# Optimization experiments

Hardware: AMD Instinct MI355X
Metric: run time of the kernel (lower is better)

## Reference

```python
import jax, jax.numpy as jnp
import numpy as np

EPS_BN = 1e-5
NEG_SLOPE = 0.2

def gat_layer(x, src, dst, N, W, a_src, a_dst, b, heads, ch, concat):
    # x: [N, Fin]; W: [Fin, heads*ch]; a_src/a_dst: [heads, ch]; b: [heads*ch] or [ch]
    xw = (x @ W).reshape(N, heads, ch)                      # [N,H,C]
    al_src = jnp.einsum('nhc,hc->nh', xw, a_src)            # [N,H]
    al_dst = jnp.einsum('nhc,hc->nh', xw, a_dst)
    e = jax.nn.leaky_relu(al_src[src] + al_dst[dst], NEG_SLOPE)  # [E,H]
    m = jax.ops.segment_max(e, dst, num_segments=N)         # segment softmax (stable)
    ee = jnp.exp(e - m[dst])
    s = jax.ops.segment_sum(ee, dst, num_segments=N)
    alpha = ee / (s[dst] + 1e-16)                            # [E,H]
    msg = xw[src] * alpha[:, :, None]                        # [E,H,C]
    out = jax.ops.segment_sum(msg, dst, num_segments=N)      # [N,H,C]
    if concat:
        return out.reshape(N, heads * ch) + b
    return out.mean(axis=1) + b

def setup_inputs():
    key = jax.random.key(0)
    ks = jax.random.split(key, 24)
    N, E, dim_in, dim_out = 20000, 320000, 256, 16
    x = jax.random.normal(ks[0], (N, dim_in), dtype=jnp.float32)
    edge_index = jax.random.randint(ks[1], (2, E), 0, N, dtype=jnp.int64)
    def glorot(k, shape):
        fan = shape[0] + shape[-1]
        return jax.random.uniform(k, shape, jnp.float32, -1.0, 1.0) * np.sqrt(6.0 / fan)
    return {
        'x': x, 'edge_index': edge_index,
        'bn_gamma': jnp.ones((dim_in,), jnp.float32),
        'bn_beta': jnp.zeros((dim_in,), jnp.float32),
        'W1': glorot(ks[2], (dim_in, 16 * 64)),
        'a1_src': glorot(ks[3], (16, 64)), 'a1_dst': glorot(ks[4], (16, 64)),
        'b1': jnp.zeros((16 * 64,), jnp.float32),
        'p1': jnp.float32(0.25),
        'W2': glorot(ks[5], (dim_in + 16 * 64, 8 * 8)),
        'a2_src': glorot(ks[6], (8, 8)), 'a2_dst': glorot(ks[7], (8, 8)),
        'b2': jnp.zeros((8 * 8,), jnp.float32),
        'p2': jnp.float32(0.25),
        'W3': glorot(ks[8], (8 * 8, 8 * dim_out)),
        'a3_src': glorot(ks[9], (8, dim_out)), 'a3_dst': glorot(ks[10], (8, dim_out)),
        'b3': jnp.zeros((dim_out,), jnp.float32),
    }

def reference(x, edge_index, bn_gamma, bn_beta, W1, a1_src, a1_dst, b1, p1,
              W2, a2_src, a2_dst, b2, p2, W3, a3_src, a3_dst, b3):
    N = x.shape[0]
    # PyG GATConv default add_self_loops=True
    loops = jnp.arange(N, dtype=edge_index.dtype)
    src = jnp.concatenate([edge_index[0], loops])
    dst = jnp.concatenate([edge_index[1], loops])
    # BatchNorm1d (training-mode batch stats)
    mu = x.mean(axis=0)
    var = x.var(axis=0)
    x_in = (x - mu) * jax.lax.rsqrt(var + EPS_BN) * bn_gamma + bn_beta
    h = gat_layer(x_in, src, dst, N, W1, a1_src, a1_dst, b1, 16, 64, True)
    h = jnp.where(h >= 0, h, p1 * h)  # PReLU
    h = gat_layer(jnp.concatenate([x_in, h], axis=1), src, dst, N, W2, a2_src, a2_dst, b2, 8, 8, True)
    h = jnp.where(h >= 0, h, p2 * h)
    h = gat_layer(h, src, dst, N, W3, a3_src, a3_dst, b3, 8, b3.shape[0], False)
    return jax.nn.log_softmax(h, axis=1)
```

## Files before the change

### kernel.cpp

```cpp
#include <hip/hip_runtime.h>
#include <math.h>

typedef unsigned int u32;
typedef unsigned short u16;
typedef u32 u32x4 __attribute__((ext_vector_type(4)));
typedef float f32x4 __attribute__((ext_vector_type(4)));

__device__ __forceinline__ u16 f2bf(float f) {
  u32 u = __builtin_bit_cast(u32, f);
  return (u16)((u + 0x7FFFu + ((u >> 16) & 1u)) >> 16);
}
__device__ __forceinline__ float bf2f(u32 lo16) {
  return __builtin_bit_cast(float, lo16 << 16);
}
__device__ __forceinline__ void mfma16(f32x4& c, const u32x4& a, const u32x4& b) {
  asm volatile("v_mfma_f32_16x16x32_bf16 %0, %1, %2, %0" : "+v"(c) : "v"(a), "v"(b));
}
__device__ __forceinline__ float lrelu(float e) { return fmaxf(e, 0.2f * e); }

__global__ void bn_stats_kernel(const float* __restrict__ x, float* __restrict__ musum,
                                float* __restrict__ sqsum, int N, int F) {
  int t = threadIdx.x;
  float s = 0.f, s2 = 0.f;
  for (int r = blockIdx.x; r < N; r += gridDim.x) {
    float v = x[(size_t)r * F + t];
    s += v;
    s2 += v * v;
  }
  atomicAdd(&musum[t], s);
  atomicAdd(&sqsum[t], s2);
}

__global__ void bn_finalize_kernel(const float* __restrict__ musum, const float* __restrict__ sqsum,
                                   const float* __restrict__ gamma, const float* __restrict__ beta,
                                   float* __restrict__ scale, float* __restrict__ shift, int N) {
  int t = threadIdx.x;
  float m = musum[t] / (float)N;
  float v = sqsum[t] / (float)N - m * m;
  float sc = gamma[t] * rsqrtf(v + 1e-5f);
  scale[t] = sc;
  shift[t] = beta[t] - m * sc;
}

__global__ void bn_apply_bf16_kernel(const float* __restrict__ x, const float* __restrict__ scale,
                                     const float* __restrict__ shift, u16* __restrict__ xin,
                                     int total, int Fmask) {
  int i = blockIdx.x * blockDim.x + threadIdx.x;
  if (i < total) {
    int c = i & Fmask;
    xin[i] = f2bf(x[i] * scale[c] + shift[c]);
  }
}

__global__ void csr_count_kernel(const int* __restrict__ ei, int E, int N, int* __restrict__ cnt) {
  int e = blockIdx.x * blockDim.x + threadIdx.x;
  int ET = E + N;
  if (e < ET) {
    int d = (e < E) ? ei[E + e] : (e - E);
    atomicAdd(&cnt[d], 1);
  }
}

__global__ __launch_bounds__(1024) void csr_scan_kernel(const int* __restrict__ cnt,
                                                        int* __restrict__ row_ptr,
                                                        int* __restrict__ cursor, int N) {
  __shared__ int part[1024];
  int t = threadIdx.x;
  int chunk = (N + 1023) / 1024;
  int lo = t * chunk;
  int hi = min(lo + chunk, N);
  int s = 0;
  for (int i = lo; i < hi; i++) s += cnt[i];
  part[t] = s;
  __syncthreads();
  for (int off = 1; off < 1024; off <<= 1) {
    int v = (t >= off) ? part[t - off] : 0;
    __syncthreads();
    part[t] += v;
    __syncthreads();
  }
  int run = (t == 0) ? 0 : part[t - 1];
  for (int i = lo; i < hi; i++) {
    row_ptr[i] = run;
    cursor[i] = run;
    run += cnt[i];
  }
  if (t == 1023) row_ptr[N] = part[1023];
}

__global__ void csr_fill_kernel(const int* __restrict__ ei, int E, int N,
                                int* __restrict__ cursor, int* __restrict__ csr_src) {
  int e = blockIdx.x * blockDim.x + threadIdx.x;
  int ET = E + N;
  if (e < ET) {
    int s, d;
    if (e < E) { s = ei[e]; d = ei[E + e]; }
    else       { s = e - E; d = s; }
    int pos = atomicAdd(&cursor[d], 1);
    csr_src[pos] = s;
  }
}

__global__ void wt_build_all(const float* __restrict__ W1, const float* __restrict__ W2,
                             const float* __restrict__ W3, u16* __restrict__ Wt1,
                             u16* __restrict__ Wt2, u16* __restrict__ Wt3) {
  const int S1 = 1024 * 256, S2 = 64 * 1280, S3 = 128 * 64;
  const int P1 = 96 * 256, P2 = 32 * 1280, P3 = 32 * 64;
  int idx = blockIdx.x * blockDim.x + threadIdx.x;
  if (idx < S1) {
    int n = idx / 256, k = idx % 256;
    Wt1[idx] = f2bf(W1[(size_t)k * 1024 + n]);
  } else if (idx < S1 + S2) {
    int i = idx - S1;
    int n = i / 1280, k = i % 1280;
    Wt2[i] = f2bf(W2[(size_t)k * 64 + n]);
  } else if (idx < S1 + S2 + S3) {
    int i = idx - S1 - S2;
    int n = i / 64, k = i % 64;
    Wt3[i] = f2bf(W3[(size_t)k * 128 + n]);
  } else if (idx < S1 + S2 + S3 + P1) {
    Wt1[S1 + (idx - S1 - S2 - S3)] = 0;
  } else if (idx < S1 + S2 + S3 + P1 + P2) {
    Wt2[S2 + (idx - S1 - S2 - S3 - P1)] = 0;
  } else if (idx < S1 + S2 + S3 + P1 + P2 + P3) {
    Wt3[S3 + (idx - S1 - S2 - S3 - P1 - P2)] = 0;
  }
}

__global__ void alfold_build(const float* __restrict__ W1, const float* __restrict__ a1s,
                             const float* __restrict__ a1d, const float* __restrict__ W2,
                             const float* __restrict__ a2s, const float* __restrict__ a2d,
                             const float* __restrict__ W3, const float* __restrict__ a3s,
                             const float* __restrict__ a3d, u16* __restrict__ Wt1,
                             u16* __restrict__ Wt2, u16* __restrict__ Wt3) {
  const int T1 = 32 * 256, T2 = 16 * 1280, T3 = 16 * 64;
  int idx = blockIdx.x * blockDim.x + threadIdx.x;
  if (idx < T1) {
    int jj = idx / 256, k = idx % 256, h = jj >> 1;
    const float* av = (jj & 1) ? a1d : a1s;
    float s = 0.f;
    for (int c = 0; c < 64; c++) s += W1[(size_t)k * 1024 + h * 64 + c] * av[h * 64 + c];
    Wt1[(size_t)(1024 + jj) * 256 + k] = f2bf(s);
  } else if (idx < T1 + T2) {
    int i = idx - T1;
    int jj = i / 1280, k = i % 1280, h = jj >> 1;
    const float* av = (jj & 1) ? a2d : a2s;
    float s = 0.f;
    for (int c = 0; c < 8; c++) s += W2[(size_t)k * 64 + h * 8 + c] * av[h * 8 + c];
    Wt2[(size_t)(64 + jj) * 1280 + k] = f2bf(s);
  } else if (idx < T1 + T2 + T3) {
    int i = idx - T1 - T2;
    int jj = i / 64, k = i % 64, h = jj >> 1;
    const float* av = (jj & 1) ? a3d : a3s;
    float s = 0.f;
    for (int c = 0; c < 16; c++) s += W3[(size_t)k * 128 + h * 16 + c] * av[h * 16 + c];
    Wt3[(size_t)(128 + jj) * 64 + k] = f2bf(s);
  }
}

template <int BM, int BN, int FM, int FN>
__global__ __launch_bounds__(256) void mfma_gemm_al(
    const u16* __restrict__ A1, const u16* __restrict__ A2, int K1, int K,
    const u16* __restrict__ Wt, u16* __restrict__ Ch, int NcH,
    float* __restrict__ als, float* __restrict__ ald, int ALN, int M) {
  constexpr int BK = 32;
  constexpr int ACH = (BM * BK) / 8;
  constexpr int BCH = (BN * BK) / 8;
  static_assert(BM == 2 * FM * 16 && BN == 2 * FN * 16, "wave grid 2x2");
  __shared__ u16 As[BM * BK];
  __shared__ u16 Bs[BN * BK];
  int t = threadIdx.x;
  int m0 = blockIdx.x * BM, n0 = blockIdx.y * BN;
  int r = t & 15;
  int g = (t >> 4) & 3;
  int wid = t >> 6;
  int wm0 = (wid >> 1) * (FM * 16);
  int wn0 = (wid & 1) * (FN * 16);
  int K8 = K >> 3;
  int K2 = K - K1;

  f32x4 acc[FM][FN] = {};
  asm volatile("s_nop 7\n\ts_nop 7" :::);

  for (int k0 = 0; k0 < K; k0 += BK) {
    const u16* Aseg;
    int sA, kl;
    if (k0 < K1) { Aseg = A1; sA = K1; kl = k0; }
    else         { Aseg = A2; sA = K2; kl = k0 - K1; }
    __syncthreads();
#pragma unroll
    for (int i = 0; i < (ACH + 255) / 256; i++) {
      int c = i * 256 + t;
      if (ACH % 256 == 0 || c < ACH) {
        int m = c >> 2, kb = c & 3;
        *(u32x4*)(As + c * 8) =
            *(const u32x4*)(Aseg + (size_t)(m0 + m) * sA + kl + kb * 8);
      }
    }
#pragma unroll
    for (int i = 0; i < (BCH + 255) / 256; i++) {
      int c = i * 256 + t;
      if (BCH % 256 == 0 || c < BCH) {
        int nn = c >> 2, kb = c & 3;
        *(u32x4*)(Bs + c * 8) =
            *(const u32x4*)(Wt + ((size_t)(n0 + nn) * K8 + (k0 >> 3) + kb) * 8);
      }
    }
    __syncthreads();
    u32x4 af[FM], bfr[FN];
#pragma unroll
    for (int fi = 0; fi < FM; fi++)
      af[fi] = *(const u32x4*)(As + ((wm0 + fi * 16 + r) * 4 + g) * 8);
#pragma unroll
    for (int fj = 0; fj < FN; fj++)
      bfr[fj] = *(const u32x4*)(Bs + ((wn0 + fj * 16 + r) * 4 + g) * 8);
#pragma unroll
    for (int fi = 0; fi < FM; fi++)
#pragma unroll
      for (int fj = 0; fj < FN; fj++) mfma16(acc[fi][fj], af[fi], bfr[fj]);
  }
  asm volatile("s_nop 7\n\ts_nop 7" :::);

#pragma unroll
  for (int fi = 0; fi < FM; fi++) {
#pragma unroll
    for (int fj = 0; fj < FN; fj++) {
#pragma unroll
      for (int v = 0; v < 4; v++) {
        int m = m0 + wm0 + fi * 16 + g * 4 + v;
        int nn = n0 + wn0 + fj * 16 + r;
        if (m < M) {
          float val = acc[fi][fj][v];
          if (nn < NcH) {
            Ch[(size_t)m * NcH + nn] = f2bf(val);
          } else {
            int j = nn - NcH;
            if (j < ALN) ((j & 1) ? ald : als)[(size_t)m * (ALN >> 1) + (j >> 1)] = val;
          }
        }
      }
    }
  }
}

__global__ __launch_bounds__(256) void gat_agg1_wave(
    const u16* __restrict__ xwh, const float* __restrict__ alsrc,
    const float* __restrict__ aldst, const int* __restrict__ row_ptr,
    const int* __restrict__ csr_src, const float* __restrict__ bias,
    const float* __restrict__ slope_p, u16* __restrict__ out, int N) {
  constexpr int U = 6;
  int wid = blockIdx.x * 4 + (threadIdx.x >> 6);
  int n = wid >> 1, q = wid & 1;
  if (n >= N) return;
  int lane = threadIdx.x & 63;
  int head = q * 8 + (lane >> 3), g = lane & 7;
  float ad = aldst[(size_t)n * 16 + head];
  int start = row_ptr[n];
  int end = row_ptr[n + 1];
  int deg = end - start;
  int endm1 = end - 1;

  float m = -1e30f, s = 0.f;
  for (int j = g; j < deg; j += 8) {
    int sj = csr_src[start + j];
    float e = lrelu(alsrc[(size_t)sj * 16 + head] + ad);
    float mn = fmaxf(m, e);
    s = s * __expf(m - mn) + __expf(e - mn);
    m = mn;
  }
#pragma unroll
  for (int st = 1; st <= 4; st <<= 1) {
    float m2 = __shfl_xor(m, st);
    float s2 = __shfl_xor(s, st);
    float mn = fmaxf(m, m2);
    s = s * __expf(m - mn) + s2 * __expf(m2 - mn);
    m = mn;
  }
  float rr = 1.f / (s + 1e-16f);

  float acc[8] = {};
  const u16* base = xwh + (size_t)q * 512 + (size_t)lane * 8;

  auto fma8 = [&](const u32x4& v, float w) {
#pragma unroll
    for (int i = 0; i < 4; i++) {
      u32 u = v[i];
      acc[2 * i] = fmaf(w, bf2f(u & 0xffffu), acc[2 * i]);
      acc[2 * i + 1] = fmaf(w, bf2f(u >> 16), acc[2 * i + 1]);
    }
  };

  int c[U];
#pragma unroll
  for (int i = 0; i < U; i++) c[i] = csr_src[min(start + i, endm1)];
  int j = 0;
  for (; j + U <= deg; j += U) {
    u32x4 v[U];
    float a[U];
#pragma unroll
    for (int i = 0; i < U; i++) v[i] = *(const u32x4*)(base + (size_t)c[i] * 1024);
#pragma unroll
    for (int i = 0; i < U; i++) a[i] = alsrc[(size_t)c[i] * 16 + head];
#pragma unroll
    for (int i = 0; i < U; i++) c[i] = csr_src[min(start + j + U + i, endm1)];
#pragma unroll
    for (int i = 0; i < U; i++) {
      float w = __expf(lrelu(a[i] + ad) - m) * rr;
      fma8(v[i], w);
    }
  }
  for (int i = 0; j < deg; j++, i++) {
    u32x4 v = *(const u32x4*)(base + (size_t)c[i] * 1024);
    float a = alsrc[(size_t)c[i] * 16 + head];
    float w = __expf(lrelu(a + ad) - m) * rr;
    fma8(v, w);
  }

  float p = slope_p[0];
  u32 ow[4];
#pragma unroll
  for (int i = 0; i < 4; i++) {
    int cc = q * 512 + lane * 8 + 2 * i;
    float v0 = acc[2 * i] + bias[cc];
    float v1 = acc[2 * i + 1] + bias[cc + 1];
    v0 = (v0 >= 0.f) ? v0 : p * v0;
    v1 = (v1 >= 0.f) ? v1 : p * v1;
    ow[i] = (u32)f2bf(v0) | ((u32)f2bf(v1) << 16);
  }
  *(u32x4*)((u32*)(out + (size_t)n * 1024 + q * 512) + lane * 4) = *(u32x4*)ow;
}

__global__ __launch_bounds__(256) void gat_agg2_wave(
    const u16* __restrict__ xwh, const float* __restrict__ alsrc,
    const float* __restrict__ aldst, const int* __restrict__ row_ptr,
    const int* __restrict__ csr_src, const float* __restrict__ bias,
    const float* __restrict__ slope_p, u16* __restrict__ out, int N) {
  constexpr int U = 8;
  int n = blockIdx.x * 4 + (threadIdx.x >> 6);
  if (n >= N) return;
  int lane = threadIdx.x & 63;
  int head = lane >> 3, g = lane & 7;
  float ad = aldst[(size_t)n * 8 + head];
  int start = row_ptr[n];
  int end = row_ptr[n + 1];
  int deg = end - start;
  int endm1 = end - 1;

  float m = -1e30f, s = 0.f;
  for (int j = g; j < deg; j += 8) {
    int sj = csr_src[start + j];
    float e = lrelu(alsrc[(size_t)sj * 8 + head] + ad);
    float mn = fmaxf(m, e);
    s = s * __expf(m - mn) + __expf(e - mn);
    m = mn;
  }
#pragma unroll
  for (int st = 1; st <= 4; st <<= 1) {
    float m2 = __shfl_xor(m, st);
    float s2 = __shfl_xor(s, st);
    float mn = fmaxf(m, m2);
    s = s * __expf(m - mn) + s2 * __expf(m2 - mn);
    m = mn;
  }
  float rr = 1.f / (s + 1e-16f);

  float acc = 0.f;
  int c[U];
#pragma unroll
  for (int i = 0; i < U; i++) c[i] = csr_src[min(start + i, endm1)];
  int j = 0;
  for (; j + U <= deg; j += U) {
    u16 v[U];
    float a[U];
#pragma unroll
    for (int i = 0; i < U; i++) v[i] = xwh[(size_t)c[i] * 64 + lane];
#pragma unroll
    for (int i = 0; i < U; i++) a[i] = alsrc[(size_t)c[i] * 8 + head];
#pragma unroll
    for (int i = 0; i < U; i++) c[i] = csr_src[min(start + j + U + i, endm1)];
#pragma unroll
    for (int i = 0; i < U; i++) {
      float w = __expf(lrelu(a[i] + ad) - m) * rr;
      acc = fmaf(w, bf2f(v[i]), acc);
    }
  }
  for (int i = 0; j < deg; j++, i++) {
    float v = bf2f(xwh[(size_t)c[i] * 64 + lane]);
    float w = __expf(lrelu(alsrc[(size_t)c[i] * 8 + head] + ad) - m) * rr;
    acc = fmaf(w, v, acc);
  }

  float p = slope_p[0];
  float v = acc + bias[lane];
  out[(size_t)n * 64 + lane] = f2bf((v >= 0.f) ? v : p * v);
}

__global__ __launch_bounds__(256) void gat_agg3_wave(
    const u16* __restrict__ xwh, const float* __restrict__ alsrc,
    const float* __restrict__ aldst, const int* __restrict__ row_ptr,
    const int* __restrict__ csr_src, const float* __restrict__ bias,
    float* __restrict__ out, int N) {
  constexpr int U = 8;
  int n = blockIdx.x * 4 + (threadIdx.x >> 6);
  if (n >= N) return;
  int lane = threadIdx.x & 63;
  int head = lane >> 3, g = lane & 7;
  float ad = aldst[(size_t)n * 8 + head];
  int start = row_ptr[n];
  int end = row_ptr[n + 1];
  int deg = end - start;
  int endm1 = end - 1;

  float m = -1e30f, s = 0.f;
  for (int j = g; j < deg; j += 8) {
    int sj = csr_src[start + j];
    float e = lrelu(alsrc[(size_t)sj * 8 + head] + ad);
    float mn = fmaxf(m, e);
    s = s * __expf(m - mn) + __expf(e - mn);
    m = mn;
  }
#pragma unroll
  for (int st = 1; st <= 4; st <<= 1) {
    float m2 = __shfl_xor(m, st);
    float s2 = __shfl_xor(s, st);
    float mn = fmaxf(m, m2);
    s = s * __expf(m - mn) + s2 * __expf(m2 - mn);
    m = mn;
  }
  float rr = 1.f / (s + 1e-16f);

  float a0 = 0.f, a1 = 0.f;
  int c[U];
#pragma unroll
  for (int i = 0; i < U; i++) c[i] = csr_src[min(start + i, endm1)];
  int j = 0;
  for (; j + U <= deg; j += U) {
    u32 v[U];
    float a[U];
#pragma unroll
    for (int i = 0; i < U; i++) v[i] = *(const u32*)(xwh + (size_t)c[i] * 128 + lane * 2);
#pragma unroll
    for (int i = 0; i < U; i++) a[i] = alsrc[(size_t)c[i] * 8 + head];
#pragma unroll
    for (int i = 0; i < U; i++) c[i] = csr_src[min(start + j + U + i, endm1)];
#pragma unroll
    for (int i = 0; i < U; i++) {
      float w = __expf(lrelu(a[i] + ad) - m) * rr;
      a0 = fmaf(w, bf2f(v[i] & 0xffffu), a0);
      a1 = fmaf(w, bf2f(v[i] >> 16), a1);
    }
  }
  for (int i = 0; j < deg; j++, i++) {
    u32 v = *(const u32*)(xwh + (size_t)c[i] * 128 + lane * 2);
    float w = __expf(lrelu(alsrc[(size_t)c[i] * 8 + head] + ad) - m) * rr;
    a0 = fmaf(w, bf2f(v & 0xffffu), a0);
    a1 = fmaf(w, bf2f(v >> 16), a1);
  }

#pragma unroll
  for (int st = 8; st <= 32; st <<= 1) {
    a0 += __shfl_xor(a0, st);
    a1 += __shfl_xor(a1, st);
  }
  int c0 = (2 * lane) & 15, c1 = (2 * lane + 1) & 15;
  float v0 = a0 * 0.125f + bias[c0];
  float v1 = a1 * 0.125f + bias[c1];
  float mx = fmaxf(v0, v1);
#pragma unroll
  for (int st = 1; st <= 4; st <<= 1) mx = fmaxf(mx, __shfl_xor(mx, st));
  float se = __expf(v0 - mx) + __expf(v1 - mx);
#pragma unroll
  for (int st = 1; st <= 4; st <<= 1) se += __shfl_xor(se, st);
  float lse = mx + logf(se);
  if (lane < 8) {
    float2 o = make_float2(v0 - lse, v1 - lse);
    *((float2*)(out + (size_t)n * 16) + lane) = o;
  }
}

extern "C" void kernel_launch(void* const* d_in, const int* in_sizes, int n_in,
                              void* d_out, int out_size, void* d_ws, size_t ws_size,
                              hipStream_t stream) {
  const float* x        = (const float*)d_in[0];
  const int*   ei       = (const int*)d_in[1];
  const float* bn_gamma = (const float*)d_in[2];
  const float* bn_beta  = (const float*)d_in[3];
  const float* W1       = (const float*)d_in[4];
  const float* a1s      = (const float*)d_in[5];
  const float* a1d      = (const float*)d_in[6];
  const float* b1       = (const float*)d_in[7];
  const float* p1       = (const float*)d_in[8];
  const float* W2       = (const float*)d_in[9];
  const float* a2s      = (const float*)d_in[10];
  const float* a2d      = (const float*)d_in[11];
  const float* b2       = (const float*)d_in[12];
  const float* p2       = (const float*)d_in[13];
  const float* W3       = (const float*)d_in[14];
  const float* a3s      = (const float*)d_in[15];
  const float* a3d      = (const float*)d_in[16];
  const float* b3       = (const float*)d_in[17];
  float* out = (float*)d_out;

  const int F  = in_sizes[2];
  const int N  = in_sizes[0] / F;
  const int E  = in_sizes[1] / 2;
  const int ET = E + N;
  const int MP = ((N + 127) / 128) * 128;

  size_t off = 0;
  auto alloc = [&](size_t bytes) -> char* {
    char* r = (char*)d_ws + off;
    off += (bytes + 255) & ~(size_t)255;
    return r;
  };
  float* musum   = (float*)alloc(F * 4);
  float* sqsum   = (float*)alloc(F * 4);
  float* scale   = (float*)alloc(F * 4);
  float* shift   = (float*)alloc(F * 4);
  int*   row_ptr = (int*)alloc((size_t)(N + 1) * 4);
  int*   cursor  = (int*)alloc((size_t)N * 4);
  int*   csr_src = (int*)alloc((size_t)ET * 4);
  float* al_s    = (float*)alloc((size_t)N * 16 * 4);
  float* al_d    = (float*)alloc((size_t)N * 16 * 4);
  u16*   Wt1     = (u16*)alloc((size_t)1152 * 256 * 2);
  u16*   Wt2     = (u16*)alloc((size_t)96 * 1280 * 2);
  u16*   Wt3     = (u16*)alloc((size_t)160 * 64 * 2);
  u16*   x_in_h  = (u16*)alloc((size_t)MP * 256 * 2);
  u16*   xw1h    = (u16*)alloc((size_t)MP * 1024 * 2);
  u16*   h1      = (u16*)alloc((size_t)MP * 1024 * 2);
  u16*   xw2h    = (u16*)alloc((size_t)MP * 64 * 2);
  u16*   h2h     = (u16*)alloc((size_t)MP * 64 * 2);
  u16*   xw3h    = (u16*)alloc((size_t)MP * 128 * 2);

  hipMemsetAsync(musum, 0, (size_t)2 * F * 4, stream);
  bn_stats_kernel<<<256, 256, 0, stream>>>(x, musum, sqsum, N, F);
  bn_finalize_kernel<<<1, F, 0, stream>>>(musum, sqsum, bn_gamma, bn_beta, scale, shift, N);
  int totalXF = N * F;
  bn_apply_bf16_kernel<<<(totalXF + 255) / 256, 256, 0, stream>>>(x, scale, shift, x_in_h,
                                                                  totalXF, F - 1);

  hipMemsetAsync(cursor, 0, (size_t)N * 4, stream);
  csr_count_kernel<<<(ET + 255) / 256, 256, 0, stream>>>(ei, E, N, cursor);
  csr_scan_kernel<<<1, 1024, 0, stream>>>(cursor, row_ptr, cursor, N);
  csr_fill_kernel<<<(ET + 255) / 256, 256, 0, stream>>>(ei, E, N, cursor, csr_src);

  {
    int total = 1024 * 256 + 64 * 1280 + 128 * 64 + 96 * 256 + 32 * 1280 + 32 * 64;
    wt_build_all<<<(total + 255) / 256, 256, 0, stream>>>(W1, W2, W3, Wt1, Wt2, Wt3);
    int tot2 = 32 * 256 + 16 * 1280 + 16 * 64;
    alfold_build<<<(tot2 + 255) / 256, 256, 0, stream>>>(W1, a1s, a1d, W2, a2s, a2d, W3, a3s, a3d,
                                                         Wt1, Wt2, Wt3);
  }

  int nblk = (N + 3) / 4;

  {
    dim3 grid(MP / 128, 9);
    mfma_gemm_al<128, 128, 4, 4><<<grid, 256, 0, stream>>>(
        x_in_h, x_in_h, 256, 256, Wt1, xw1h, 1024, al_s, al_d, 32, N);
    gat_agg1_wave<<<(2 * N + 3) / 4, 256, 0, stream>>>(xw1h, al_s, al_d, row_ptr, csr_src, b1, p1,
                                                       h1, N);
  }

  {
    dim3 grid((N + 63) / 64, 1);
    mfma_gemm_al<64, 96, 2, 3><<<grid, 256, 0, stream>>>(
        x_in_h, h1, 256, 1280, Wt2, xw2h, 64, al_s, al_d, 16, N);
    gat_agg2_wave<<<nblk, 256, 0, stream>>>(xw2h, al_s, al_d, row_ptr, csr_src, b2, p2, h2h, N);
  }

  {
    dim3 grid((N + 63) / 64, 1);
    mfma_gemm_al<64, 160, 2, 5><<<grid, 256, 0, stream>>>(
        h2h, h2h, 64, 64, Wt3, xw3h, 128, al_s, al_d, 16, N);
    gat_agg3_wave<<<nblk, 256, 0, stream>>>(xw3h, al_s, al_d, row_ptr, csr_src, b3, out, N);
  }
}
```

Baseline: 343.7 us.

## Transpose attention logits to head-major and split layer-1 aggregation per head across XCDs

Attention logit arrays are now stored head-major ([head][node] with padded stride) instead of node-major, so per-head gathers touch a compact per-head vector. Layer-1 aggregation is restructured so each wave handles one node and one head (64 channels), with block IDs mapped so each XCD handles the same head. The intent is to keep per-head xw slices and logits resident in each XCD's L2 instead of gathering full 2KB rows. The cost is more waves, each recomputing the softmax and reloading the CSR indices, plus narrower 2-byte gathers per lane instead of 16-byte vector loads.

```diff
diff --git a/kernel.cpp b/kernel.cpp
--- a/kernel.cpp
+++ b/kernel.cpp
@@ -162,7 +162,7 @@
 __global__ __launch_bounds__(256) void mfma_gemm_al(
     const u16* __restrict__ A1, const u16* __restrict__ A2, int K1, int K,
     const u16* __restrict__ Wt, u16* __restrict__ Ch, int NcH,
-    float* __restrict__ als, float* __restrict__ ald, int ALN, int M) {
+    float* __restrict__ als, float* __restrict__ ald, int ALN, int ALP, int M) {
   constexpr int BK = 32;
   constexpr int ACH = (BM * BK) / 8;
   constexpr int BCH = (BN * BK) / 8;
@@ -235,7 +235,7 @@
             Ch[(size_t)m * NcH + nn] = f2bf(val);
           } else {
             int j = nn - NcH;
-            if (j < ALN) ((j & 1) ? ald : als)[(size_t)m * (ALN >> 1) + (j >> 1)] = val;
+            if (j < ALN) ((j & 1) ? ald : als)[(size_t)(j >> 1) * ALP + m] = val;
           }
         }
       }
@@ -243,27 +243,97 @@
   }
 }
 
-__global__ __launch_bounds__(256) void gat_agg1_wave(
+__global__ __launch_bounds__(256) void gat_agg1_hslice(
     const u16* __restrict__ xwh, const float* __restrict__ alsrc,
     const float* __restrict__ aldst, const int* __restrict__ row_ptr,
     const int* __restrict__ csr_src, const float* __restrict__ bias,
-    const float* __restrict__ slope_p, u16* __restrict__ out, int N) {
+    const float* __restrict__ slope_p, u16* __restrict__ out, int N, int ALP, int NB) {
   constexpr int U = 6;
-  int wid = blockIdx.x * 4 + (threadIdx.x >> 6);
-  int n = wid >> 1, q = wid & 1;
+  int b = blockIdx.x;
+  int xcd = b & 7;
+  int seq = b >> 3;
+  int phase = seq / NB;
+  int nodeblk = seq - phase * NB;
+  int h = xcd + (phase << 3);
+  int n = nodeblk * 4 + (threadIdx.x >> 6);
   if (n >= N) return;
   int lane = threadIdx.x & 63;
-  int head = q * 8 + (lane >> 3), g = lane & 7;
-  float ad = aldst[(size_t)n * 16 + head];
+  const float* alh = alsrc + (size_t)h * ALP;
+  float ad = aldst[(size_t)h * ALP + n];
   int start = row_ptr[n];
   int end = row_ptr[n + 1];
   int deg = end - start;
   int endm1 = end - 1;
 
   float m = -1e30f, s = 0.f;
+  for (int j = lane; j < deg; j += 64) {
+    float e = lrelu(alh[csr_src[start + j]] + ad);
+    float mn = fmaxf(m, e);
+    s = s * __expf(m - mn) + __expf(e - mn);
+    m = mn;
+  }
+#pragma unroll
+  for (int st = 1; st <= 32; st <<= 1) {
+    float m2 = __shfl_xor(m, st);
+    float s2 = __shfl_xor(s, st);
+    float mn = fmaxf(m, m2);
+    s = s * __expf(m - mn) + s2 * __expf(m2 - mn);
+    m = mn;
+  }
+  float rr = 1.f / (s + 1e-16f);
+
+  const u16* base = xwh + (size_t)h * 64 + lane;
+  float acc = 0.f;
+  int c[U];
+#pragma unroll
+  for (int i = 0; i < U; i++) c[i] = csr_src[min(start + i, endm1)];
+  int j = 0;
+  for (; j + U <= deg; j += U) {
+    u16 v[U];
+    float a[U];
+#pragma unroll
+    for (int i = 0; i < U; i++) v[i] = base[(size_t)c[i] * 1024];
+#pragma unroll
+    for (int i = 0; i < U; i++) a[i] = alh[c[i]];
+#pragma unroll
+    for (int i = 0; i < U; i++) c[i] = csr_src[min(start + j + U + i, endm1)];
+#pragma unroll
+    for (int i = 0; i < U; i++) {
+      float w = __expf(lrelu(a[i] + ad) - m) * rr;
+      acc = fmaf(w, bf2f(v[i]), acc);
+    }
+  }
+  for (int i = 0; j < deg; j++, i++) {
+    float w = __expf(lrelu(alh[c[i]] + ad) - m) * rr;
+    acc = fmaf(w, bf2f(base[(size_t)c[i] * 1024]), acc);
+  }
+
+  float p = slope_p[0];
+  int cc = h * 64 + lane;
+  float v = acc + bias[cc];
+  out[(size_t)n * 1024 + cc] = f2bf((v >= 0.f) ? v : p * v);
+}
+
+__global__ __launch_bounds__(256) void gat_agg2_wave(
+    const u16* __restrict__ xwh, const float* __restrict__ alsrc,
+    const float* __restrict__ aldst, const int* __restrict__ row_ptr,
+    const int* __restrict__ csr_src, const float* __restrict__ bias,
+    const float* __restrict__ slope_p, u16* __restrict__ out, int N, int ALP) {
+  constexpr int U = 8;
+  int n = blockIdx.x * 4 + (threadIdx.x >> 6);
+  if (n >= N) return;
+  int lane = threadIdx.x & 63;
+  int head = lane >> 3, g = lane & 7;
+  const float* alh = alsrc + (size_t)head * ALP;
+  float ad = aldst[(size_t)head * ALP + n];
+  int start = row_ptr[n];
+  int end = row_ptr[n + 1];
+  int deg = end - start;
+  int endm1 = end - 1;
+
+  float m = -1e30f, s = 0.f;
   for (int j = g; j < deg; j += 8) {
-    int sj = csr_src[start + j];
-    float e = lrelu(alsrc[(size_t)sj * 16 + head] + ad);
+    float e = lrelu(alh[csr_src[start + j]] + ad);
     float mn = fmaxf(m, e);
     s = s * __expf(m - mn) + __expf(e - mn);
     m = mn;
@@ -278,69 +348,49 @@
   }
   float rr = 1.f / (s + 1e-16f);
 
-  float acc[8] = {};
-  const u16* base = xwh + (size_t)q * 512 + (size_t)lane * 8;
-
-  auto fma8 = [&](const u32x4& v, float w) {
-#pragma unroll
-    for (int i = 0; i < 4; i++) {
-      u32 u = v[i];
-      acc[2 * i] = fmaf(w, bf2f(u & 0xffffu), acc[2 * i]);
-      acc[2 * i + 1] = fmaf(w, bf2f(u >> 16), acc[2 * i + 1]);
-    }
-  };
-
+  float acc = 0.f;
   int c[U];
 #pragma unroll
   for (int i = 0; i < U; i++) c[i] = csr_src[min(start + i, endm1)];
   int j = 0;
   for (; j + U <= deg; j += U) {
-    u32x4 v[U];
+    u16 v[U];
     float a[U];
 #pragma unroll
-    for (int i = 0; i < U; i++) v[i] = *(const u32x4*)(base + (size_t)c[i] * 1024);
-#pragma unroll
-    for (int i = 0; i < U; i++) a[i] = alsrc[(size_t)c[i] * 16 + head];
+    for (int i = 0; i < U; i++) v[i] = xwh[(size_t)c[i] * 64 + lane];
+#pragma unroll
+    for (int i = 0; i < U; i++) a[i] = alh[c[i]];
 #pragma unroll
     for (int i = 0; i < U; i++) c[i] = csr_src[min(start + j + U + i, endm1)];
 #pragma unroll
     for (int i = 0; i < U; i++) {
       float w = __expf(lrelu(a[i] + ad) - m) * rr;
-      fma8(v[i], w);
+      acc = fmaf(w, bf2f(v[i]), acc);
     }
   }
   for (int i = 0; j < deg; j++, i++) {
-    u32x4 v = *(const u32x4*)(base + (size_t)c[i] * 1024);
-    float a = alsrc[(size_t)c[i] * 16 + head];
-    float w = __expf(lrelu(a + ad) - m) * rr;
-    fma8(v, w);
+    float v = bf2f(xwh[(size_t)c[i] * 64 + lane]);
+    float w = __expf(lrelu(alh[c[i]] + ad) - m) * rr;
+    acc = fmaf(w, v, acc);
   }
 
   float p = slope_p[0];
-  u32 ow[4];
-#pragma unroll
-  for (int i = 0; i < 4; i++) {
-    int cc = q * 512 + lane * 8 + 2 * i;
-    float v0 = acc[2 * i] + bias[cc];
-    float v1 = acc[2 * i + 1] + bias[cc + 1];
-    v0 = (v0 >= 0.f) ? v0 : p * v0;
-    v1 = (v1 >= 0.f) ? v1 : p * v1;
-    ow[i] = (u32)f2bf(v0) | ((u32)f2bf(v1) << 16);
-  }
-  *(u32x4*)((u32*)(out + (size_t)n * 1024 + q * 512) + lane * 4) = *(u32x4*)ow;
-}
-
-__global__ __launch_bounds__(256) void gat_agg2_wave(
+  float v = acc + bias[lane];
+  out[(size_t)n * 64 + lane] = f2bf((v >= 0.f) ? v : p * v);
+}
+
+__global__ __launch_bounds__(256) void gat_agg3_wave(
     const u16* __restrict__ xwh, const float* __restrict__ alsrc,
     const float* __restrict__ aldst, const int* __restrict__ row_ptr,
     const int* __restrict__ csr_src, const float* __restrict__ bias,
-    const float* __restrict__ slope_p, u16* __restrict__ out, int N) {
+    float* __restrict__ out, int N, int ALP) {
   constexpr int U = 8;
   int n = blockIdx.x * 4 + (threadIdx.x >> 6);
   if (n >= N) return;
   int lane = threadIdx.x & 63;
   int head = lane >> 3, g = lane & 7;
-  float ad = aldst[(size_t)n * 8 + head];
+  const float* alh = alsrc + (size_t)head * ALP;
+  float ad = aldst[(size_t)head * ALP + n];
   int start = row_ptr[n];
   int end = row_ptr[n + 1];
   int deg = end - start;
@@ -348,8 +398,7 @@
 
   float m = -1e30f, s = 0.f;
   for (int j = g; j < deg; j += 8) {
-    int sj = csr_src[start + j];
-    float e = lrelu(alsrc[(size_t)sj * 8 + head] + ad);
+    float e = lrelu(alh[csr_src[start + j]] + ad);
     float mn = fmaxf(m, e);
     s = s * __expf(m - mn) + __expf(e - mn);
     m = mn;
@@ -364,71 +413,6 @@
   }
   float rr = 1.f / (s + 1e-16f);
 
-  float acc = 0.f;
-  int c[U];
-#pragma unroll
-  for (int i = 0; i < U; i++) c[i] = csr_src[min(start + i, endm1)];
-  int j = 0;
-  for (; j + U <= deg; j += U) {
-    u16 v[U];
-    float a[U];
-#pragma unroll
-    for (int i = 0; i < U; i++) v[i] = xwh[(size_t)c[i] * 64 + lane];
-#pragma unroll
-    for (int i = 0; i < U; i++) a[i] = alsrc[(size_t)c[i] * 8 + head];
-#pragma unroll
-    for (int i = 0; i < U; i++) c[i] = csr_src[min(start + j + U + i, endm1)];
-#pragma unroll
-    for (int i = 0; i < U; i++) {
-      float w = __expf(lrelu(a[i] + ad) - m) * rr;
-      acc = fmaf(w, bf2f(v[i]), acc);
-    }
-  }
-  for (int i = 0; j < deg; j++, i++) {
-    float v = bf2f(xwh[(size_t)c[i] * 64 + lane]);
-    float w = __expf(lrelu(alsrc[(size_t)c[i] * 8 + head] + ad) - m) * rr;
-    acc = fmaf(w, v, acc);
-  }
-
-  float p = slope_p[0];
-  float v = acc + bias[lane];
-  out[(size_t)n * 64 + lane] = f2bf((v >= 0.f) ? v : p * v);
-}
-
-__global__ __launch_bounds__(256) void gat_agg3_wave(
-    const u16* __restrict__ xwh, const float* __restrict__ alsrc,
-    const float* __restrict__ aldst, const int* __restrict__ row_ptr,
-    const int* __restrict__ csr_src, const float* __restrict__ bias,
-    float* __restrict__ out, int N) {
-  constexpr int U = 8;
-  int n = blockIdx.x * 4 + (threadIdx.x >> 6);
-  if (n >= N) return;
-  int lane = threadIdx.x & 63;
-  int head = lane >> 3, g = lane & 7;
-  float ad = aldst[(size_t)n * 8 + head];
-  int start = row_ptr[n];
-  int end = row_ptr[n + 1];
-  int deg = end - start;
-  int endm1 = end - 1;
-
-  float m = -1e30f, s = 0.f;
-  for (int j = g; j < deg; j += 8) {
-    int sj = csr_src[start + j];
-    float e = lrelu(alsrc[(size_t)sj * 8 + head] + ad);
-    float mn = fmaxf(m, e);
-    s = s * __expf(m - mn) + __expf(e - mn);
-    m = mn;
-  }
-#pragma unroll
-  for (int st = 1; st <= 4; st <<= 1) {
-    float m2 = __shfl_xor(m, st);
-    float s2 = __shfl_xor(s, st);
-    float mn = fmaxf(m, m2);
-    s = s * __expf(m - mn) + s2 * __expf(m2 - mn);
-    m = mn;
-  }
-  float rr = 1.f / (s + 1e-16f);
-
   float a0 = 0.f, a1 = 0.f;
   int c[U];
 #pragma unroll
@@ -440,7 +424,7 @@
 #pragma unroll
     for (int i = 0; i < U; i++) v[i] = *(const u32*)(xwh + (size_t)c[i] * 128 + lane * 2);
 #pragma unroll
-    for (int i = 0; i < U; i++) a[i] = alsrc[(size_t)c[i] * 8 + head];
+    for (int i = 0; i < U; i++) a[i] = alh[c[i]];
 #pragma unroll
     for (int i = 0; i < U; i++) c[i] = csr_src[min(start + j + U + i, endm1)];
 #pragma unroll
@@ -452,7 +436,7 @@
   }
   for (int i = 0; j < deg; j++, i++) {
     u32 v = *(const u32*)(xwh + (size_t)c[i] * 128 + lane * 2);
-    float w = __expf(lrelu(alsrc[(size_t)c[i] * 8 + head] + ad) - m) * rr;
+    float w = __expf(lrelu(alh[c[i]] + ad) - m) * rr;
     a0 = fmaf(w, bf2f(v & 0xffffu), a0);
     a1 = fmaf(w, bf2f(v >> 16), a1);
   }
@@ -520,8 +504,8 @@
   int*   row_ptr = (int*)alloc((size_t)(N + 1) * 4);
   int*   cursor  = (int*)alloc((size_t)N * 4);
   int*   csr_src = (int*)alloc((size_t)ET * 4);
-  float* al_s    = (float*)alloc((size_t)N * 16 * 4);
-  float* al_d    = (float*)alloc((size_t)N * 16 * 4);
+  float* al_s    = (float*)alloc((size_t)16 * MP * 4);
+  float* al_d    = (float*)alloc((size_t)16 * MP * 4);
   u16*   Wt1     = (u16*)alloc((size_t)1152 * 256 * 2);
   u16*   Wt2     = (u16*)alloc((size_t)96 * 1280 * 2);
   u16*   Wt3     = (u16*)alloc((size_t)160 * 64 * 2);
@@ -557,22 +541,22 @@
   {
     dim3 grid(MP / 128, 9);
     mfma_gemm_al<128, 128, 4, 4><<<grid, 256, 0, stream>>>(
-        x_in_h, x_in_h, 256, 256, Wt1, xw1h, 1024, al_s, al_d, 32, N);
-    gat_agg1_wave<<<(2 * N + 3) / 4, 256, 0, stream>>>(xw1h, al_s, al_d, row_ptr, csr_src, b1, p1,
-                                                       h1, N);
+        x_in_h, x_in_h, 256, 256, Wt1, xw1h, 1024, al_s, al_d, 32, MP, N);
+    gat_agg1_hslice<<<8 * nblk * 2, 256, 0, stream>>>(xw1h, al_s, al_d, row_ptr, csr_src, b1, p1,
+                                                      h1, N, MP, nblk);
   }
 
   {
     dim3 grid((N + 63) / 64, 1);
     mfma_gemm_al<64, 96, 2, 3><<<grid, 256, 0, stream>>>(
-        x_in_h, h1, 256, 1280, Wt2, xw2h, 64, al_s, al_d, 16, N);
-    gat_agg2_wave<<<nblk, 256, 0, stream>>>(xw2h, al_s, al_d, row_ptr, csr_src, b2, p2, h2h, N);
+        x_in_h, h1, 256, 1280, Wt2, xw2h, 64, al_s, al_d, 16, MP, N);
+    gat_agg2_wave<<<nblk, 256, 0, stream>>>(xw2h, al_s, al_d, row_ptr, csr_src, b2, p2, h2h, N, MP);
   }
 
   {
     dim3 grid((N + 63) / 64, 1);
     mfma_gemm_al<64, 160, 2, 5><<<grid, 256, 0, stream>>>(
-        h2h, h2h, 64, 64, Wt3, xw3h, 128, al_s, al_d, 16, N);
-    gat_agg3_wave<<<nblk, 256, 0, stream>>>(xw3h, al_s, al_d, row_ptr, csr_src, b3, out, N);
-  }
-}
+        h2h, h2h, 64, 64, Wt3, xw3h, 128, al_s, al_d, 16, MP, N);
+    gat_agg3_wave<<<nblk, 256, 0, stream>>>(xw3h, al_s, al_d, row_ptr, csr_src, b3, out, N, MP);
+  }
+}
```

New measurement: 484.3 us. 1.41x slower.
